# Performance work log

Hardware: AMD Instinct MI355X
Metric: run time of the kernel (lower is better)

The kernel has to match this reference:

```python
import jax, jax.numpy as jnp
import numpy as np

VOCAB = 82
EMBED = 256
HIDDEN = 128
PAD = 0


def setup_inputs() -> dict:
    key = jax.random.key(0)
    ks = jax.random.split(key, 7)
    B, T = 256, 512
    sqrt_k = (1.0 / HIDDEN) ** 0.5
    tokens = jax.random.randint(ks[0], (B, T), 0, VOCAB)
    emb = jax.random.normal(ks[1], (VOCAB, EMBED), dtype=jnp.float32)
    emb = emb.at[PAD].set(0.0)  # padding_idx row is zero
    W_f = jax.random.uniform(ks[2], (HIDDEN, HIDDEN + EMBED), minval=-sqrt_k, maxval=sqrt_k)
    W_c = jax.random.uniform(ks[3], (HIDDEN, HIDDEN + EMBED), minval=-sqrt_k, maxval=sqrt_k)
    W_o = jax.random.uniform(ks[4], (HIDDEN, HIDDEN + EMBED), minval=-sqrt_k, maxval=sqrt_k)
    clf_W = jax.random.uniform(ks[5], (VOCAB, HIDDEN), minval=-sqrt_k, maxval=sqrt_k)
    clf_b = jax.random.uniform(ks[6], (VOCAB,), minval=-sqrt_k, maxval=sqrt_k)
    return {"batch_reviews": tokens, "emb": emb, "W_f": W_f, "W_c": W_c,
            "W_o": W_o, "clf_W": clf_W, "clf_b": clf_b}


def reference(batch_reviews, emb, W_f, W_c, W_o, clf_W, clf_b):
    # embed: [B, T, E]
    data = emb[batch_reviews]
    B, T, E = data.shape
    # scan over time: carry = (h, c); emit gate signals per step
    xs = jnp.swapaxes(data, 0, 1)  # [T, B, E]

    def step(carry, x_t):
        h, c = carry
        hx = jnp.concatenate([h, x_t], axis=1)            # [B, H+E]
        f = jax.nn.sigmoid(hx @ W_f.T)                    # [B, H]
        o = jax.nn.sigmoid(hx @ W_o.T)
        c_tilde = jnp.tanh(hx @ W_c.T)
        next_c = f * c + (1.0 - f) * c_tilde              # coupled forget/input gate
        next_h = o * jnp.tanh(next_c)
        return (next_h, next_c), (f, o, c_tilde)

    h0 = jnp.zeros((B, HIDDEN), dtype=data.dtype)
    c0 = jnp.zeros((B, HIDDEN), dtype=data.dtype)
    (h_T, c_T), (f_all, o_all, ct_all) = jax.lax.scan(step, (h0, c0), xs)
    logits = h_T @ clf_W.T + clf_b                        # [B, VOCAB]
    # gate stacks are [T, B, H], matching torch's per-step list of gate tuples
    return logits, f_all, o_all, ct_all
```

## Files before the change

kernel.cpp:

```cpp
#include <hip/hip_runtime.h>

#define VOCAB  82
#define EMBED  256
#define HIDDEN 128
#define BATCH  256
#define SEQ    512
#define KX     (HIDDEN + EMBED)

__device__ __align__(16) float Gv_buf[VOCAB * 3 * HIDDEN];

__device__ __forceinline__ float fast_sigmoid(float x) {
    return 1.f / (1.f + __expf(-x));
}
__device__ __forceinline__ float fast_tanh(float x) {
    x = fminf(fmaxf(x, -15.f), 15.f);
    float e = __expf(2.f * x);
    return (e - 1.f) / (e + 1.f);
}

__global__ __launch_bounds__(384, 2)
void gv_prologue(const float* __restrict__ emb,
                 const float* __restrict__ Wf,
                 const float* __restrict__ Wc,
                 const float* __restrict__ Wo) {
    const int v   = blockIdx.x;
    const int tid = threadIdx.x;
    const int g   = tid >> 7;
    const int r   = tid & 127;

    __shared__ __align__(16) float e_lds[EMBED];
    if (tid < EMBED) e_lds[tid] = emb[(size_t)v * EMBED + tid];
    __syncthreads();

    const float* Wg = (g == 0) ? Wf : (g == 1) ? Wo : Wc;
    const float4* wr = (const float4*)(Wg + (size_t)r * KX + HIDDEN);
    const float4* ev = (const float4*)e_lds;
    float a0 = 0.f, a1 = 0.f, a2 = 0.f, a3 = 0.f;
#pragma unroll
    for (int i = 0; i < EMBED / 4; ++i) {
        float4 w4 = wr[i];
        float4 e4 = ev[i];
        a0 += w4.x * e4.x;
        a1 += w4.y * e4.y;
        a2 += w4.z * e4.z;
        a3 += w4.w * e4.w;
    }
    Gv_buf[(size_t)v * (3 * HIDDEN) + tid] = (a0 + a1) + (a2 + a3);
}

__global__ __launch_bounds__(384, 2)
void lstm_main(const int* __restrict__ tokens,
               const float* __restrict__ Wf,
               const float* __restrict__ Wc,
               const float* __restrict__ Wo,
               const float* __restrict__ clfW,
               const float* __restrict__ clfb,
               float* __restrict__ out) {
    const int b   = blockIdx.x;
    const int tid = threadIdx.x;
    const int g   = tid >> 7;
    const int r   = tid & 127;

    __shared__ __align__(16) float h_lds[HIDDEN];
    __shared__ float gates[3][HIDDEN];
    __shared__ int   tok[SEQ];

    const float* Wg = (g == 0) ? Wf : (g == 1) ? Wo : Wc;
    const float4* wr4 = (const float4*)(Wg + (size_t)r * KX);
    float w[HIDDEN];
#pragma unroll
    for (int i = 0; i < HIDDEN / 4; ++i) {
        float4 w4 = wr4[i];
        w[4 * i + 0] = w4.x;
        w[4 * i + 1] = w4.y;
        w[4 * i + 2] = w4.z;
        w[4 * i + 3] = w4.w;
    }

    for (int i = tid; i < SEQ; i += 384) tok[i] = tokens[(size_t)b * SEQ + i];
    if (tid < HIDDEN) h_lds[tid] = 0.f;
    float c = 0.f;
    __syncthreads();

    const size_t GATE0 = (size_t)BATCH * VOCAB;
    const size_t GSZ   = (size_t)SEQ * BATCH * HIDDEN;
    float* gout = out + GATE0 + (size_t)g * GSZ + (size_t)b * HIDDEN + r;

    float val = 0.f;
    for (int t = 0; t < SEQ; ++t) {
        const int tk = tok[t];
        const float gx = Gv_buf[tk * (3 * HIDDEN) + tid];

        const float4* h4 = (const float4*)h_lds;
        float a0 = 0.f, a1 = 0.f, a2 = 0.f, a3 = 0.f;
#pragma unroll
        for (int i = 0; i < HIDDEN / 4; ++i) {
            float4 hv = h4[i];
            a0 += w[4 * i + 0] * hv.x;
            a1 += w[4 * i + 1] * hv.y;
            a2 += w[4 * i + 2] * hv.z;
            a3 += w[4 * i + 3] * hv.w;
        }
        const float pre = (a0 + a1) + (a2 + a3) + gx;
        val = (g == 2) ? fast_tanh(pre) : fast_sigmoid(pre);
        gates[g][r] = val;
        __syncthreads();
        if (tid < HIDDEN) {
            const float f  = gates[0][r];
            const float o  = gates[1][r];
            const float ct = gates[2][r];
            c = f * c + (1.f - f) * ct;
            h_lds[r] = o * fast_tanh(c);
        }
        __syncthreads();
        gout[(size_t)t * (BATCH * HIDDEN)] = val;
    }

    if (tid < VOCAB) {
        const float4* cw = (const float4*)(clfW + (size_t)tid * HIDDEN);
        const float4* h4 = (const float4*)h_lds;
        float a0 = 0.f, a1 = 0.f, a2 = 0.f, a3 = 0.f;
#pragma unroll
        for (int i = 0; i < HIDDEN / 4; ++i) {
            float4 wv = cw[i];
            float4 hv = h4[i];
            a0 += wv.x * hv.x;
            a1 += wv.y * hv.y;
            a2 += wv.z * hv.z;
            a3 += wv.w * hv.w;
        }
        out[(size_t)b * VOCAB + tid] = (a0 + a1) + (a2 + a3) + clfb[tid];
    }
}

extern "C" void kernel_launch(void* const* d_in, const int* in_sizes, int n_in,
                              void* d_out, int out_size, void* d_ws, size_t ws_size,
                              hipStream_t stream) {
    const int*   tokens = (const int*)  d_in[0];
    const float* emb    = (const float*)d_in[1];
    const float* Wf     = (const float*)d_in[2];
    const float* Wc     = (const float*)d_in[3];
    const float* Wo     = (const float*)d_in[4];
    const float* clfW   = (const float*)d_in[5];
    const float* clfb   = (const float*)d_in[6];
    float*       out    = (float*)d_out;

    gv_prologue<<<VOCAB, 384, 0, stream>>>(emb, Wf, Wc, Wo);
    lstm_main<<<BATCH, 384, 0, stream>>>(tokens, Wf, Wc, Wo, clfW, clfb, out);
}
```

Measured before the change: 640.6 us.

## Split hidden-state dot products across quad lanes and reduce with DPP shuffles

The recurrent matvec is repartitioned so each hidden unit is handled by 4 lanes, each owning a 32-wide slice of h for all three gates, with partial sums combined via DPP quad reductions. Every lane then computes the cell update redundantly. This removes the gates shared-memory exchange and one of the two barriers per timestep, and double-buffers h with padded segments to avoid bank conflicts. The prologue is also split into one block per (vocab, gate) pair. The cost is that each lane now does work for all three gates, and the fourth lane of each quad idles on gate output stores.

```diff
diff --git a/kernel.cpp b/kernel.cpp
--- a/kernel.cpp
+++ b/kernel.cpp
@@ -6,6 +6,7 @@
 #define BATCH  256
 #define SEQ    512
 #define KX     (HIDDEN + EMBED)
+#define SEG    36
 
 __device__ __align__(16) float Gv_buf[VOCAB * 3 * HIDDEN];
 
@@ -17,19 +18,25 @@
     float e = __expf(2.f * x);
     return (e - 1.f) / (e + 1.f);
 }
+__device__ __forceinline__ float quad_sum(float x) {
+    int y1 = __builtin_amdgcn_mov_dpp(__float_as_int(x), 0xB1, 0xF, 0xF, true);
+    x = x + __int_as_float(y1);
+    int y2 = __builtin_amdgcn_mov_dpp(__float_as_int(x), 0x4E, 0xF, 0xF, true);
+    return x + __int_as_float(y2);
+}
 
-__global__ __launch_bounds__(384, 2)
+__global__ __launch_bounds__(128, 2)
 void gv_prologue(const float* __restrict__ emb,
                  const float* __restrict__ Wf,
                  const float* __restrict__ Wc,
                  const float* __restrict__ Wo) {
-    const int v   = blockIdx.x;
-    const int tid = threadIdx.x;
-    const int g   = tid >> 7;
-    const int r   = tid & 127;
+    const int g = blockIdx.x % 3;
+    const int v = blockIdx.x / 3;
+    const int r = threadIdx.x;
 
     __shared__ __align__(16) float e_lds[EMBED];
-    if (tid < EMBED) e_lds[tid] = emb[(size_t)v * EMBED + tid];
+    e_lds[r]       = emb[(size_t)v * EMBED + r];
+    e_lds[r + 128] = emb[(size_t)v * EMBED + r + 128];
     __syncthreads();
 
     const float* Wg = (g == 0) ? Wf : (g == 1) ? Wo : Wc;
@@ -45,10 +52,10 @@
         a2 += w4.z * e4.z;
         a3 += w4.w * e4.w;
     }
-    Gv_buf[(size_t)v * (3 * HIDDEN) + tid] = (a0 + a1) + (a2 + a3);
+    Gv_buf[(size_t)v * 384 + g * 128 + r] = (a0 + a1) + (a2 + a3);
 }
 
-__global__ __launch_bounds__(384, 2)
+__global__ __launch_bounds__(512, 2)
 void lstm_main(const int* __restrict__ tokens,
                const float* __restrict__ Wf,
                const float* __restrict__ Wc,
@@ -58,78 +65,80 @@
                float* __restrict__ out) {
     const int b   = blockIdx.x;
     const int tid = threadIdx.x;
-    const int g   = tid >> 7;
-    const int r   = tid & 127;
+    const int q   = tid & 3;
+    const int r   = tid >> 2;
 
-    __shared__ __align__(16) float h_lds[HIDDEN];
-    __shared__ float gates[3][HIDDEN];
-    __shared__ int   tok[SEQ];
+    __shared__ __align__(16) float hbuf[2][4 * SEG];
+    __shared__ int tok[SEQ];
 
-    const float* Wg = (g == 0) ? Wf : (g == 1) ? Wo : Wc;
-    const float4* wr4 = (const float4*)(Wg + (size_t)r * KX);
-    float w[HIDDEN];
+    float4 wf[8], wo[8], wc[8];
+    {
+        const float4* pf = (const float4*)(Wf + (size_t)r * KX + q * 32);
+        const float4* po = (const float4*)(Wo + (size_t)r * KX + q * 32);
+        const float4* pc = (const float4*)(Wc + (size_t)r * KX + q * 32);
 #pragma unroll
-    for (int i = 0; i < HIDDEN / 4; ++i) {
-        float4 w4 = wr4[i];
-        w[4 * i + 0] = w4.x;
-        w[4 * i + 1] = w4.y;
-        w[4 * i + 2] = w4.z;
-        w[4 * i + 3] = w4.w;
+        for (int i = 0; i < 8; ++i) { wf[i] = pf[i]; wo[i] = po[i]; wc[i] = pc[i]; }
     }
 
-    for (int i = tid; i < SEQ; i += 384) tok[i] = tokens[(size_t)b * SEQ + i];
-    if (tid < HIDDEN) h_lds[tid] = 0.f;
+    tok[tid] = tokens[(size_t)b * SEQ + tid];
+    if (tid < HIDDEN) hbuf[0][(tid >> 5) * SEG + (tid & 31)] = 0.f;
     float c = 0.f;
     __syncthreads();
 
     const size_t GATE0 = (size_t)BATCH * VOCAB;
     const size_t GSZ   = (size_t)SEQ * BATCH * HIDDEN;
-    float* gout = out + GATE0 + (size_t)g * GSZ + (size_t)b * HIDDEN + r;
+    float* gout = out + GATE0 + (size_t)q * GSZ + (size_t)b * HIDDEN + r;
 
-    float val = 0.f;
     for (int t = 0; t < SEQ; ++t) {
+        const int p  = t & 1;
         const int tk = tok[t];
-        const float gx = Gv_buf[tk * (3 * HIDDEN) + tid];
+        const float gx = (q < 3) ? Gv_buf[tk * 384 + q * 128 + r] : 0.f;
 
-        const float4* h4 = (const float4*)h_lds;
-        float a0 = 0.f, a1 = 0.f, a2 = 0.f, a3 = 0.f;
+        const float4* hv4 = (const float4*)&hbuf[p][q * SEG];
+        float pf = 0.f, po = 0.f, pc = 0.f;
 #pragma unroll
-        for (int i = 0; i < HIDDEN / 4; ++i) {
-            float4 hv = h4[i];
-            a0 += w[4 * i + 0] * hv.x;
-            a1 += w[4 * i + 1] * hv.y;
-            a2 += w[4 * i + 2] * hv.z;
-            a3 += w[4 * i + 3] * hv.w;
+        for (int i = 0; i < 8; ++i) {
+            float4 h4 = hv4[i];
+            pf += wf[i].x * h4.x; pf += wf[i].y * h4.y;
+            pf += wf[i].z * h4.z; pf += wf[i].w * h4.w;
+            po += wo[i].x * h4.x; po += wo[i].y * h4.y;
+            po += wo[i].z * h4.z; po += wo[i].w * h4.w;
+            pc += wc[i].x * h4.x; pc += wc[i].y * h4.y;
+            pc += wc[i].z * h4.z; pc += wc[i].w * h4.w;
         }
-        const float pre = (a0 + a1) + (a2 + a3) + gx;
-        val = (g == 2) ? fast_tanh(pre) : fast_sigmoid(pre);
-        gates[g][r] = val;
+        pf += (q == 0) ? gx : 0.f;
+        po += (q == 1) ? gx : 0.f;
+        pc += (q == 2) ? gx : 0.f;
+
+        const float pre_f = quad_sum(pf);
+        const float pre_o = quad_sum(po);
+        const float pre_c = quad_sum(pc);
+
+        const float f  = fast_sigmoid(pre_f);
+        const float o  = fast_sigmoid(pre_o);
+        const float ct = fast_tanh(pre_c);
+        c = f * c + (1.f - f) * ct;
+        const float h = o * fast_tanh(c);
+
+        if (q == 0) hbuf[1 - p][(r >> 5) * SEG + (r & 31)] = h;
         __syncthreads();
-        if (tid < HIDDEN) {
-            const float f  = gates[0][r];
-            const float o  = gates[1][r];
-            const float ct = gates[2][r];
-            c = f * c + (1.f - f) * ct;
-            h_lds[r] = o * fast_tanh(c);
-        }
-        __syncthreads();
-        gout[(size_t)t * (BATCH * HIDDEN)] = val;
+        const float sval = (q == 0) ? f : (q == 1) ? o : ct;
+        if (q < 3) gout[(size_t)t * (BATCH * HIDDEN)] = sval;
     }
 
-    if (tid < VOCAB) {
-        const float4* cw = (const float4*)(clfW + (size_t)tid * HIDDEN);
-        const float4* h4 = (const float4*)h_lds;
-        float a0 = 0.f, a1 = 0.f, a2 = 0.f, a3 = 0.f;
+    if (tid < 4 * VOCAB) {
+        const int v = tid >> 2;
+        const float4* cw  = (const float4*)(clfW + (size_t)v * HIDDEN + q * 32);
+        const float4* hv4 = (const float4*)&hbuf[0][q * SEG];
+        float a = 0.f;
 #pragma unroll
-        for (int i = 0; i < HIDDEN / 4; ++i) {
-            float4 wv = cw[i];
-            float4 hv = h4[i];
-            a0 += wv.x * hv.x;
-            a1 += wv.y * hv.y;
-            a2 += wv.z * hv.z;
-            a3 += wv.w * hv.w;
+        for (int i = 0; i < 8; ++i) {
+            float4 w4 = cw[i];
+            float4 h4 = hv4[i];
+            a += w4.x * h4.x + w4.y * h4.y + w4.z * h4.z + w4.w * h4.w;
         }
-        out[(size_t)b * VOCAB + tid] = (a0 + a1) + (a2 + a3) + clfb[tid];
+        a = quad_sum(a);
+        if (q == 0) out[(size_t)b * VOCAB + v] = a + clfb[v];
     }
 }
 
@@ -145,6 +154,6 @@
     const float* clfb   = (const float*)d_in[6];
     float*       out    = (float*)d_out;
 
-    gv_prologue<<<VOCAB, 384, 0, stream>>>(emb, Wf, Wc, Wo);
-    lstm_main<<<BATCH, 384, 0, stream>>>(tokens, Wf, Wc, Wo, clfW, clfb, out);
+    gv_prologue<<<3 * VOCAB, 128, 0, stream>>>(emb, Wf, Wc, Wo);
+    lstm_main<<<BATCH, 512, 0, stream>>>(tokens, Wf, Wc, Wo, clfW, clfb, out);
 }
```

Result: faster. 563.3 us (-12.1%).
